# Optimization experiments

Hardware: AMD Instinct MI355X
Metric: run time of the kernel (lower is better)

The kernel has to match this reference:

```python
import jax, jax.numpy as jnp
import numpy as np

B, S, D = 16, 2048, 256

def setup_inputs() -> dict:
    key = jax.random.key(0)
    ks = jax.random.split(key, 7)
    scale = 1.0 / np.sqrt(D)
    return {
        "x": jax.random.normal(ks[0], (B, S, D), dtype=jnp.float32),
        "Wq": jax.random.normal(ks[1], (D, D), dtype=jnp.float32) * scale,
        "bq": jax.random.normal(ks[2], (D,), dtype=jnp.float32) * 0.01,
        "Wk": jax.random.normal(ks[3], (D, D), dtype=jnp.float32) * scale,
        "bk": jax.random.normal(ks[4], (D,), dtype=jnp.float32) * 0.01,
        "Wv": jax.random.normal(ks[5], (D, D), dtype=jnp.float32) * scale,
        "bv": jax.random.normal(ks[6], (D,), dtype=jnp.float32) * 0.01,
    }

def reference(x, Wq, bq, Wk, bk, Wv, bv):
    # q,k,v: [B,S,D]
    q = x @ Wq + bq
    k = x @ Wk + bk
    v = x @ Wv + bv
    inv_sqrt_d = jnp.asarray(1.0 / np.sqrt(x.shape[-1]), dtype=x.dtype)
    energy = jnp.einsum('bqd,bkd->bqk', q, k) * inv_sqrt_d  # [B,S,S]
    attn = jax.nn.softmax(energy, axis=-1)
    weighted = jnp.einsum('bqk,bkd->bqd', attn, v)  # [B,S,D]
    return weighted.sum(axis=1)  # [B,D]
```

## Files before the change

kernel.cpp:

```cpp
#include <hip/hip_runtime.h>
#include <hip/hip_bf16.h>

typedef __bf16 bf16_t;
typedef bf16_t bf16x8 __attribute__((ext_vector_type(8)));
typedef float  f32x4  __attribute__((ext_vector_type(4)));

constexpr int S = 2048, D = 256;


__device__ __forceinline__ float fast_exp2(float x) {
    return __builtin_amdgcn_exp2f(x);
}

__global__ void wt_kernel(const float* __restrict__ Wq, const float* __restrict__ Wk,
                          bf16_t* __restrict__ wtf) {
    int idx = blockIdx.x * 256 + threadIdx.x;
    int w    = idx >> 13;
    int rem  = idx & 8191;
    int nt   = rem >> 9;
    int rem2 = rem & 511;
    int ks   = rem2 >> 6;
    int lane = rem2 & 63;
    int lm = lane & 15, lg = lane >> 4;
    const float* Wsrc = (w == 0) ? Wq : Wk;
    int col = nt * 16 + lm, krow = ks * 32 + lg * 8;
    bf16x8 o;
#pragma unroll
    for (int j = 0; j < 8; j++) o[j] = (bf16_t)Wsrc[(krow + j) * 256 + col];
    *(bf16x8*)(wtf + (size_t)idx * 8) = o;
}

__global__ __launch_bounds__(256) void proj_kernel(
    const float* __restrict__ x, const bf16_t* __restrict__ wtf,
    const float* __restrict__ bq, const float* __restrict__ bk,
    bf16_t* __restrict__ qo, bf16_t* __restrict__ ko) {
    __shared__ bf16_t sb_all[4][4480];
    int w    = blockIdx.y;
    int tid  = threadIdx.x;
    int wave = tid >> 6, lane = tid & 63, lm = lane & 15, lg = lane >> 4;
    int m0   = blockIdx.x * 128;
    const bf16_t* wb   = wtf + w * 65536;
    const float*  bias = (w == 0) ? bq : bk;

    f32x4 acc[2][16];
#pragma unroll
    for (int s = 0; s < 2; s++)
#pragma unroll
        for (int nt = 0; nt < 16; nt++) acc[s][nt] = f32x4{0.f, 0.f, 0.f, 0.f};

    const float* xr0 = x + (size_t)(m0 + wave * 32 + lm) * 256 + lg * 8;
    const float* xr1 = xr0 + 16 * 256;

    for (int ks = 0; ks < 8; ks++) {
        bf16x8 af[2];
        {
            float4 a0 = *(const float4*)(xr0 + ks * 32);
            float4 a1 = *(const float4*)(xr0 + ks * 32 + 4);
            float4 b0 = *(const float4*)(xr1 + ks * 32);
            float4 b1 = *(const float4*)(xr1 + ks * 32 + 4);
            af[0][0] = (bf16_t)a0.x; af[0][1] = (bf16_t)a0.y;
            af[0][2] = (bf16_t)a0.z; af[0][3] = (bf16_t)a0.w;
            af[0][4] = (bf16_t)a1.x; af[0][5] = (bf16_t)a1.y;
            af[0][6] = (bf16_t)a1.z; af[0][7] = (bf16_t)a1.w;
            af[1][0] = (bf16_t)b0.x; af[1][1] = (bf16_t)b0.y;
            af[1][2] = (bf16_t)b0.z; af[1][3] = (bf16_t)b0.w;
            af[1][4] = (bf16_t)b1.x; af[1][5] = (bf16_t)b1.y;
            af[1][6] = (bf16_t)b1.z; af[1][7] = (bf16_t)b1.w;
        }
#pragma unroll
        for (int nt = 0; nt < 16; nt++) {
            bf16x8 bfr = *(const bf16x8*)(wb + (size_t)(nt * 8 + ks) * 512 + lane * 8);
            acc[0][nt] = __builtin_amdgcn_mfma_f32_16x16x32_bf16(af[0], bfr, acc[0][nt], 0, 0, 0);
            acc[1][nt] = __builtin_amdgcn_mfma_f32_16x16x32_bf16(af[1], bfr, acc[1][nt], 0, 0, 0);
        }
    }

    bf16_t* sb = sb_all[wave];
    int bglob = m0 >> 11;
    bf16_t* dst = (w == 0) ? qo : ko;
#pragma unroll
    for (int s = 0; s < 2; s++) {
#pragma unroll
        for (int nt = 0; nt < 16; nt++) {
            int col = nt * 16 + lm;
            float bval = bias[col];
#pragma unroll
            for (int r = 0; r < 4; r++)
                sb[(lg * 4 + r) * 280 + col] = (bf16_t)(acc[s][nt][r] + bval);
        }
        int qb = ((m0 & 2047) >> 4) + wave * 2 + s;
#pragma unroll
        for (int ks = 0; ks < 8; ks++) {
            bf16x8 v8 = *(const bf16x8*)&sb[lm * 280 + ks * 32 + lg * 8];
            *(bf16x8*)(dst + ((size_t)((bglob * 128 + qb) * 8 + ks)) * 512 + lane * 8) = v8;
        }
    }
}

template <int PASS>
__global__ __launch_bounds__(512, 2) void attn_pass(
    const bf16_t* __restrict__ q, const bf16_t* __restrict__ kmat,
    float* __restrict__ lpart, float* __restrict__ wpart) {
    __shared__ bf16_t kst[2][16384];
    __shared__ bf16_t wacc[8][512];

    int tid  = threadIdx.x;
    int wave = tid >> 6, lane = tid & 63, lm = lane & 15, lg = lane >> 4;
    int i    = blockIdx.x;
    int idx2 = i >> 3;
    int qt   = idx2 & 3;
    int kh   = (idx2 >> 2) & 3;
    int b    = (i & 7) * 2 + (idx2 >> 4);

    bf16x8 af[4][8];
#pragma unroll
    for (int s = 0; s < 4; s++) {
        const bf16_t* qb = q + ((size_t)((b * 128 + qt * 32 + wave * 4 + s) * 8)) * 512;
#pragma unroll
        for (int ks = 0; ks < 8; ks++)
            af[s][ks] = *(const bf16x8*)(qb + ks * 512 + lane * 8);
    }

    float rinv[4][4];
    if (PASS == 2) {
#pragma unroll
        for (int s = 0; s < 4; s++)
#pragma unroll
            for (int r = 0; r < 4; r++) {
                int row = qt * 512 + wave * 64 + s * 16 + lg * 4 + r;
                float l = 0.f;
#pragma unroll
                for (int k2 = 0; k2 < 4; k2++)
                    l += lpart[(size_t)(k2 * 16 + b) * 2048 + row];
                rinv[s][r] = 1.0f / l;
            }
    }

    float lsum[4][4];
#pragma unroll
    for (int s = 0; s < 4; s++)
#pragma unroll
        for (int r = 0; r < 4; r++) lsum[s][r] = 0.f;

    constexpr float SCL = 0.0625f * 1.44269504f;
    const bf16_t* kb_base = kmat + (size_t)(b * 128 + kh * 32) * 4096;

    bf16x8 stg[4];
#pragma unroll
    for (int u = 0; u < 4; u++)
        stg[u] = *(const bf16x8*)(kb_base + (size_t)(u * 512 + tid) * 8);

    for (int t = 0; t < 8; t++) {
        int p = t & 1;
#pragma unroll
        for (int u = 0; u < 4; u++)
            *(bf16x8*)&kst[p][(u * 512 + tid) * 8] = stg[u];
        if (t < 7) {
#pragma unroll
            for (int u = 0; u < 4; u++)
                stg[u] = *(const bf16x8*)(kb_base + (size_t)(t + 1) * 16384 + (u * 512 + tid) * 8);
        }
        __syncthreads();

#pragma unroll
        for (int h = 0; h < 2; h++) {
            f32x4 sacc[4][2];
#pragma unroll
            for (int s = 0; s < 4; s++) {
                sacc[s][0] = f32x4{0.f, 0.f, 0.f, 0.f};
                sacc[s][1] = f32x4{0.f, 0.f, 0.f, 0.f};
            }
#pragma unroll
            for (int ks = 0; ks < 8; ks++) {
                bf16x8 b0 = *(const bf16x8*)&kst[p][((h * 2 + 0) * 8 + ks) * 512 + lane * 8];
                bf16x8 b1 = *(const bf16x8*)&kst[p][((h * 2 + 1) * 8 + ks) * 512 + lane * 8];
#pragma unroll
                for (int s = 0; s < 4; s++) {
                    sacc[s][0] = __builtin_amdgcn_mfma_f32_16x16x32_bf16(af[s][ks], b0, sacc[s][0], 0, 0, 0);
                    sacc[s][1] = __builtin_amdgcn_mfma_f32_16x16x32_bf16(af[s][ks], b1, sacc[s][1], 0, 0, 0);
                }
            }
            if (PASS == 1) {
#pragma unroll
                for (int s = 0; s < 4; s++)
#pragma unroll
                    for (int j = 0; j < 2; j++)
#pragma unroll
                        for (int r = 0; r < 4; r++)
                            lsum[s][r] += fast_exp2(sacc[s][j][r] * SCL);
            } else {
#pragma unroll
                for (int j = 0; j < 2; j++) {
                    float wv = 0.f;
#pragma unroll
                    for (int s = 0; s < 4; s++)
#pragma unroll
                        for (int r = 0; r < 4; r++)
                            wv += fast_exp2(sacc[s][j][r] * SCL) * rinv[s][r];
                    wv += __shfl_xor(wv, 16);
                    wv += __shfl_xor(wv, 32);
                    if (lg == 0) wacc[wave][t * 64 + (h * 2 + j) * 16 + lm] = (bf16_t)wv;
                }
            }
        }
    }

    if (PASS == 1) {
#pragma unroll
        for (int s = 0; s < 4; s++)
#pragma unroll
            for (int r = 0; r < 4; r++) {
                float v2 = lsum[s][r];
                v2 += __shfl_xor(v2, 1);
                v2 += __shfl_xor(v2, 2);
                v2 += __shfl_xor(v2, 4);
                v2 += __shfl_xor(v2, 8);
                if (lm == 0) {
                    int row = qt * 512 + wave * 64 + s * 16 + lg * 4 + r;
                    lpart[(size_t)(kh * 16 + b) * 2048 + row] = v2;
                }
            }
    } else {
        __syncthreads();
        float sum = 0.f;
#pragma unroll
        for (int w2 = 0; w2 < 8; w2++) sum += (float)wacc[w2][tid];
        wpart[(size_t)(qt * 16 + b) * 2048 + kh * 512 + tid] = sum;
    }
}

__global__ __launch_bounds__(256) void xsum_kernel(
    const float* __restrict__ wpart, const float* __restrict__ x,
    float* __restrict__ gpart) {
    __shared__ float ldsw[128];
    int b = blockIdx.x >> 4, kseg = blockIdx.x & 15, tid = threadIdx.x;
    if (tid < 128) {
        int key = kseg * 128 + tid;
        float s = 0.f;
#pragma unroll
        for (int qt = 0; qt < 4; qt++) s += wpart[(size_t)(qt * 16 + b) * 2048 + key];
        ldsw[tid] = s;
    }
    __syncthreads();
    const float* xb = x + ((size_t)b * 2048 + kseg * 128) * 256;
    float acc = 0.f;
#pragma unroll 8
    for (int t = 0; t < 128; t++) acc += ldsw[t] * xb[(size_t)t * 256 + tid];
    gpart[(size_t)(kseg * 16 + b) * 256 + tid] = acc;
}

__global__ __launch_bounds__(256) void final_kernel(
    const float* __restrict__ gpart, const float* __restrict__ Wv,
    const float* __restrict__ bv, float* __restrict__ out) {
    __shared__ float yl[256];
    int b = blockIdx.x, tid = threadIdx.x;
    float s = 0.f;
#pragma unroll
    for (int ks = 0; ks < 16; ks++) s += gpart[(size_t)(ks * 16 + b) * 256 + tid];
    yl[tid] = s;
    __syncthreads();
    float acc = 0.f;
#pragma unroll 4
    for (int c = 0; c < 256; c++) acc += yl[c] * Wv[c * 256 + tid];
    out[b * 256 + tid] = acc + 2048.0f * bv[tid];
}

extern "C" void kernel_launch(void* const* d_in, const int* in_sizes, int n_in,
                              void* d_out, int out_size, void* d_ws, size_t ws_size,
                              hipStream_t stream) {
    const float* x  = (const float*)d_in[0];
    const float* Wq = (const float*)d_in[1];
    const float* bq = (const float*)d_in[2];
    const float* Wk = (const float*)d_in[3];
    const float* bk = (const float*)d_in[4];
    const float* Wv = (const float*)d_in[5];
    const float* bv = (const float*)d_in[6];
    float* out = (float*)d_out;

    char* ws = (char*)d_ws;
    bf16_t* wtf   = (bf16_t*)(ws);
    bf16_t* q     = (bf16_t*)(ws + 262144);
    bf16_t* kmat  = (bf16_t*)(ws + 17039360);
    float*  lpart = (float*) (ws + 33816576);
    float*  wpart = (float*) (ws + 34340864);
    float*  gpart = (float*) (ws + 34865152);

    wt_kernel<<<dim3(64), dim3(256), 0, stream>>>(Wq, Wk, wtf);
    proj_kernel<<<dim3(256, 2), dim3(256), 0, stream>>>(x, wtf, bq, bk, q, kmat);
    attn_pass<1><<<dim3(256), dim3(512), 0, stream>>>(q, kmat, lpart, wpart);
    attn_pass<2><<<dim3(256), dim3(512), 0, stream>>>(q, kmat, lpart, wpart);
    xsum_kernel<<<dim3(256), dim3(256), 0, stream>>>(wpart, x, gpart);
    final_kernel<<<dim3(16), dim3(256), 0, stream>>>(gpart, Wv, bv, out);
}
```

Before: 191.3 us.

## Retile projection kernel with LDS-staged weights and 2x2 wave tiling

The projection GEMM now stages half of the pre-swizzled bf16 weight matrix in shared memory and splits each block's output into a 2x2 wave grid of 64x64 tiles, doubling the grid to 512x2 blocks. Each wave preloads its whole A fragment (4 row tiles by 8 k-steps) into registers, and B fragments now come from LDS instead of global/L2. The aim is more reuse per fragment and more parallel blocks. In exchange it uses more registers and 64KB+ of LDS per block, which may limit occupancy, and each x row is now read by two blocks.

```diff
diff --git a/kernel.cpp b/kernel.cpp
--- a/kernel.cpp
+++ b/kernel.cpp
@@ -30,69 +30,82 @@
     *(bf16x8*)(wtf + (size_t)idx * 8) = o;
 }
 
-__global__ __launch_bounds__(256) void proj_kernel(
+__global__ __launch_bounds__(256, 2) void proj_kernel(
     const float* __restrict__ x, const bf16_t* __restrict__ wtf,
     const float* __restrict__ bq, const float* __restrict__ bk,
     bf16_t* __restrict__ qo, bf16_t* __restrict__ ko) {
-    __shared__ bf16_t sb_all[4][4480];
+    __shared__ bf16_t bst[32768];
+    __shared__ bf16_t sb_all[4][1152];
     int w    = blockIdx.y;
     int tid  = threadIdx.x;
     int wave = tid >> 6, lane = tid & 63, lm = lane & 15, lg = lane >> 4;
-    int m0   = blockIdx.x * 128;
+    int rowb = blockIdx.x >> 1;
+    int colh = blockIdx.x & 1;
+    int rowg = wave >> 1, colg = wave & 1;
     const bf16_t* wb   = wtf + w * 65536;
     const float*  bias = (w == 0) ? bq : bk;
 
-    f32x4 acc[2][16];
-#pragma unroll
-    for (int s = 0; s < 2; s++)
-#pragma unroll
-        for (int nt = 0; nt < 16; nt++) acc[s][nt] = f32x4{0.f, 0.f, 0.f, 0.f};
-
-    const float* xr0 = x + (size_t)(m0 + wave * 32 + lm) * 256 + lg * 8;
-    const float* xr1 = xr0 + 16 * 256;
-
+    {
+        const bf16_t* src = wb + (size_t)colh * 32768;
+#pragma unroll
+        for (int u = 0; u < 16; u++) {
+            int c = u * 256 + tid;
+            *(bf16x8*)&bst[(size_t)c * 8] = *(const bf16x8*)(src + (size_t)c * 8);
+        }
+    }
+
+    int m0 = rowb * 128 + rowg * 64;
+    bf16x8 af[4][8];
+#pragma unroll
+    for (int s = 0; s < 4; s++) {
+        const float* xr = x + (size_t)(m0 + s * 16 + lm) * 256 + lg * 8;
+#pragma unroll
+        for (int ks = 0; ks < 8; ks++) {
+            float4 a0 = *(const float4*)(xr + ks * 32);
+            float4 a1 = *(const float4*)(xr + ks * 32 + 4);
+            af[s][ks][0] = (bf16_t)a0.x; af[s][ks][1] = (bf16_t)a0.y;
+            af[s][ks][2] = (bf16_t)a0.z; af[s][ks][3] = (bf16_t)a0.w;
+            af[s][ks][4] = (bf16_t)a1.x; af[s][ks][5] = (bf16_t)a1.y;
+            af[s][ks][6] = (bf16_t)a1.z; af[s][ks][7] = (bf16_t)a1.w;
+        }
+    }
+    __syncthreads();
+
+    f32x4 acc[4][4];
+#pragma unroll
+    for (int s = 0; s < 4; s++)
+#pragma unroll
+        for (int nt = 0; nt < 4; nt++) acc[s][nt] = f32x4{0.f, 0.f, 0.f, 0.f};
+#pragma unroll
     for (int ks = 0; ks < 8; ks++) {
-        bf16x8 af[2];
-        {
-            float4 a0 = *(const float4*)(xr0 + ks * 32);
-            float4 a1 = *(const float4*)(xr0 + ks * 32 + 4);
-            float4 b0 = *(const float4*)(xr1 + ks * 32);
-            float4 b1 = *(const float4*)(xr1 + ks * 32 + 4);
-            af[0][0] = (bf16_t)a0.x; af[0][1] = (bf16_t)a0.y;
-            af[0][2] = (bf16_t)a0.z; af[0][3] = (bf16_t)a0.w;
-            af[0][4] = (bf16_t)a1.x; af[0][5] = (bf16_t)a1.y;
-            af[0][6] = (bf16_t)a1.z; af[0][7] = (bf16_t)a1.w;
-            af[1][0] = (bf16_t)b0.x; af[1][1] = (bf16_t)b0.y;
-            af[1][2] = (bf16_t)b0.z; af[1][3] = (bf16_t)b0.w;
-            af[1][4] = (bf16_t)b1.x; af[1][5] = (bf16_t)b1.y;
-            af[1][6] = (bf16_t)b1.z; af[1][7] = (bf16_t)b1.w;
-        }
-#pragma unroll
-        for (int nt = 0; nt < 16; nt++) {
-            bf16x8 bfr = *(const bf16x8*)(wb + (size_t)(nt * 8 + ks) * 512 + lane * 8);
-            acc[0][nt] = __builtin_amdgcn_mfma_f32_16x16x32_bf16(af[0], bfr, acc[0][nt], 0, 0, 0);
-            acc[1][nt] = __builtin_amdgcn_mfma_f32_16x16x32_bf16(af[1], bfr, acc[1][nt], 0, 0, 0);
+#pragma unroll
+        for (int nt = 0; nt < 4; nt++) {
+            bf16x8 bfr = *(const bf16x8*)&bst[(size_t)(((colg * 4 + nt) * 8 + ks) * 512) + lane * 8];
+#pragma unroll
+            for (int s = 0; s < 4; s++)
+                acc[s][nt] = __builtin_amdgcn_mfma_f32_16x16x32_bf16(af[s][ks], bfr, acc[s][nt], 0, 0, 0);
         }
     }
 
     bf16_t* sb = sb_all[wave];
     int bglob = m0 >> 11;
     bf16_t* dst = (w == 0) ? qo : ko;
-#pragma unroll
-    for (int s = 0; s < 2; s++) {
-#pragma unroll
-        for (int nt = 0; nt < 16; nt++) {
-            int col = nt * 16 + lm;
-            float bval = bias[col];
+    int c0 = colh * 128 + colg * 64;
+#pragma unroll
+    for (int s = 0; s < 4; s++) {
+#pragma unroll
+        for (int nt = 0; nt < 4; nt++) {
+            int colloc = nt * 16 + lm;
+            float bval = bias[c0 + colloc];
 #pragma unroll
             for (int r = 0; r < 4; r++)
-                sb[(lg * 4 + r) * 280 + col] = (bf16_t)(acc[s][nt][r] + bval);
-        }
-        int qb = ((m0 & 2047) >> 4) + wave * 2 + s;
-#pragma unroll
-        for (int ks = 0; ks < 8; ks++) {
-            bf16x8 v8 = *(const bf16x8*)&sb[lm * 280 + ks * 32 + lg * 8];
-            *(bf16x8*)(dst + ((size_t)((bglob * 128 + qb) * 8 + ks)) * 512 + lane * 8) = v8;
+                sb[(lg * 4 + r) * 72 + colloc] = (bf16_t)(acc[s][nt][r] + bval);
+        }
+        int qb = ((m0 & 2047) >> 4) + s;
+#pragma unroll
+        for (int kk = 0; kk < 2; kk++) {
+            bf16x8 v8 = *(const bf16x8*)&sb[lm * 72 + kk * 32 + lg * 8];
+            *(bf16x8*)(dst + ((size_t)((bglob * 128 + qb) * 8 + (c0 >> 5) + kk)) * 512 + lane * 8) = v8;
         }
     }
 }
@@ -286,7 +299,7 @@
     float*  gpart = (float*) (ws + 34865152);
 
     wt_kernel<<<dim3(64), dim3(256), 0, stream>>>(Wq, Wk, wtf);
-    proj_kernel<<<dim3(256, 2), dim3(256), 0, stream>>>(x, wtf, bq, bk, q, kmat);
+    proj_kernel<<<dim3(512, 2), dim3(256), 0, stream>>>(x, wtf, bq, bk, q, kmat);
     attn_pass<1><<<dim3(256), dim3(512), 0, stream>>>(q, kmat, lpart, wpart);
     attn_pass<2><<<dim3(256), dim3(512), 0, stream>>>(q, kmat, lpart, wpart);
     xsum_kernel<<<dim3(256), dim3(256), 0, stream>>>(wpart, x, gpart);
```

After: 211.6 us. 1.11x slower.
